# Performance work log

Measured on AMD Instinct MI355X. Metric: run time of the kernel, lower is better.

The kernel has to match this reference:

```python
import jax, jax.numpy as jnp
import numpy as np

RBF_START = 0.0
RBF_END = 10.0
RBF_STEPS = 64
OUT_SIZE = 64
ENERGY_SCALE = 0.1
P, L, R = 8, 128, 1024
COORD_SCALE = 5.0  # spread coords so pair distances span the 0-10 RBF range


def setup_inputs() -> dict:
    key = jax.random.key(0)
    k1, k2, k3, k4 = jax.random.split(key, 4)
    return {
        "lig_feat": jax.random.normal(k1, (L, RBF_STEPS, OUT_SIZE), dtype=jnp.float32),
        "rec_feat": jax.random.normal(k2, (R, RBF_STEPS, OUT_SIZE), dtype=jnp.float32),
        "lig_coords": jax.random.normal(k3, (P, L, 3), dtype=jnp.float32) * COORD_SCALE,
        "rec_coords": jax.random.normal(k4, (R, 3), dtype=jnp.float32) * COORD_SCALE,
    }


def reference(lig_feat, rec_feat, lig_coords, rec_coords):
    # attention coefficients: contract feature axis f -> [L, R, E]
    atn_coefs = jnp.einsum("lef,ref->lre", lig_feat, rec_feat)
    # pairwise distances for every pose: [P, L, R]
    diff = lig_coords[:, :, None, :] - rec_coords[None, None, :, :]
    dists = jnp.sqrt(jnp.sum(diff * diff, axis=-1))
    # RBF expansion: [P, L, R, E]
    mu = jnp.linspace(RBF_START, RBF_END, RBF_STEPS, dtype=jnp.float32)
    sigma = (RBF_START - RBF_END) / RBF_STEPS
    rbfs = jnp.exp(-(((dists[..., None] - mu) / sigma) ** 2))
    # attention-weighted energy per pose: [P]
    Us = jnp.einsum("plre,lre->p", rbfs, atn_coefs) * ENERGY_SCALE
    return Us
```

## Files before the change

kernel.cpp:

```cpp
#include <hip/hip_runtime.h>
#include <math.h>

#define Lc 128
#define Rc 1024
#define Pc 8
#define Ec 64
#define Fc 64

#define CSCALE   7.68718341623328f
#define MU_STEP  0.15873015873015873f
#define MUC      (MU_STEP * CSCALE)

#define BM 32
#define BN 32
#define EC 8
#define NBLKM ((Lc/BM)*(Rc/BN)*(Ec/EC))

typedef __attribute__((ext_vector_type(8))) short short8;
typedef __attribute__((ext_vector_type(4))) float f32x4;

__device__ __forceinline__ unsigned short bf16_rn(float x) {
    unsigned int u = __float_as_uint(x);
    u += 0x7FFF + ((u >> 16) & 1);
    return (unsigned short)(u >> 16);
}
__device__ __forceinline__ unsigned int hipack(float x0, float x1) {
    return (__float_as_uint(x0) >> 16) | (__float_as_uint(x1) & 0xFFFF0000u);
}
__device__ __forceinline__ unsigned int lopack(float x0, float x1) {
    float r0 = x0 - __uint_as_float(__float_as_uint(x0) & 0xFFFF0000u);
    float r1 = x1 - __uint_as_float(__float_as_uint(x1) & 0xFFFF0000u);
    return ((unsigned int)bf16_rn(r1) << 16) | (unsigned int)bf16_rn(r0);
}

__global__ __launch_bounds__(256, 2)
void ff_mfma(const float* __restrict__ lig_feat,
             const float* __restrict__ rec_feat,
             const float* __restrict__ lig_coords,
             const float* __restrict__ rec_coords,
             float* __restrict__ partial)
{
    __shared__ __align__(16) unsigned short stg[2][2][32][16][8];
    __shared__ float lcs[Pc][96];
    __shared__ float rcs[96];
    __shared__ float wred[4][Pc];

    const int tid  = threadIdx.x;
    const int lane = tid & 63;
    const int w    = tid >> 6;
    const int n16  = lane & 15;
    const int kg   = lane >> 4;
    const int sr   = w >> 1;
    const int sc   = w & 1;

    const int bid = blockIdx.x;
    const int loc = bid >> 3;
    const int rt  = (bid & 7) * 4 + (loc & 3);
    const int lt  = (loc >> 2) & 3;
    const int ez  = loc >> 4;
    const int r0  = rt * BN;
    const int l0  = lt * BM;
    const int e0  = ez * EC;

    for (int i = tid; i < Pc * 96; i += 256) {
        int p = i / 96, q = i - p * 96;
        lcs[p][q] = lig_coords[p * (Lc * 3) + l0 * 3 + q];
    }
    if (tid < 96) rcs[tid] = rec_coords[r0 * 3 + tid];
    __syncthreads();

    float dsc[Pc][4];
    {
        const int rb = (sc * 16 + n16) * 3;
        const float rx = rcs[rb], ry = rcs[rb + 1], rz = rcs[rb + 2];
        #pragma unroll
        for (int reg = 0; reg < 4; ++reg) {
            const int lb = (sr * 16 + kg * 4 + reg) * 3;
            #pragma unroll
            for (int p = 0; p < Pc; ++p) {
                float dx = lcs[p][lb]     - rx;
                float dy = lcs[p][lb + 1] - ry;
                float dz = lcs[p][lb + 2] - rz;
                dsc[p][reg] = sqrtf(dx * dx + dy * dy + dz * dz) * CSCALE;
            }
        }
    }

    const int half = tid >> 7;
    const int srow = (tid >> 2) & 31;
    const int fq   = tid & 3;
    const float* sbase = (half ? rec_feat + (size_t)(r0 + srow) * (Ec * Fc)
                               : lig_feat + (size_t)(l0 + srow) * (Ec * Fc)) + fq * 16;

    float4 pf[4];
    auto ld = [&](int e) {
        #pragma unroll
        for (int j = 0; j < 4; ++j)
            pf[j] = *(const float4*)(sbase + (size_t)e * Fc + j * 4);
    };
    auto cw = [&](int nb) {
        uint4 H0, H1, L0, L1;
        H0.x = hipack(pf[0].x, pf[0].y); H0.y = hipack(pf[0].z, pf[0].w);
        H0.z = hipack(pf[1].x, pf[1].y); H0.w = hipack(pf[1].z, pf[1].w);
        H1.x = hipack(pf[2].x, pf[2].y); H1.y = hipack(pf[2].z, pf[2].w);
        H1.z = hipack(pf[3].x, pf[3].y); H1.w = hipack(pf[3].z, pf[3].w);
        L0.x = lopack(pf[0].x, pf[0].y); L0.y = lopack(pf[0].z, pf[0].w);
        L0.z = lopack(pf[1].x, pf[1].y); L0.w = lopack(pf[1].z, pf[1].w);
        L1.x = lopack(pf[2].x, pf[2].y); L1.y = lopack(pf[2].z, pf[2].w);
        L1.z = lopack(pf[3].x, pf[3].y); L1.w = lopack(pf[3].z, pf[3].w);
        const int sm = srow & 15;
        *(uint4*)&stg[nb][half][srow][(fq * 2)         ^ sm][0] = H0;
        *(uint4*)&stg[nb][half][srow][(fq * 2 + 1)     ^ sm][0] = H1;
        *(uint4*)&stg[nb][half][srow][(8 + fq * 2)     ^ sm][0] = L0;
        *(uint4*)&stg[nb][half][srow][(8 + fq * 2 + 1) ^ sm][0] = L1;
    };

    ld(e0);
    cw(0);
    ld(e0 + 1);

    float us[Pc];
    #pragma unroll
    for (int p = 0; p < Pc; ++p) us[p] = 0.f;

    const int Arow = sr * 16 + n16;
    const int Brow = sc * 16 + n16;
#define RD(hf, rowv, slot) (*(const short8*)&stg[cur][hf][rowv][(slot) ^ ((rowv) & 15)][0])

    for (int t = 0; t < EC; ++t) {
        __syncthreads();
        const int cur = t & 1;

        f32x4 acc = {0.f, 0.f, 0.f, 0.f};
        {
            short8 a0 = RD(0, Arow, kg);
            short8 b0 = RD(1, Brow, kg);
            acc = __builtin_amdgcn_mfma_f32_16x16x32_bf16(a0, b0, acc, 0, 0, 0);
            short8 a1 = RD(0, Arow, 8 + kg);
            acc = __builtin_amdgcn_mfma_f32_16x16x32_bf16(a1, b0, acc, 0, 0, 0);
            short8 b1 = RD(1, Brow, 8 + kg);
            acc = __builtin_amdgcn_mfma_f32_16x16x32_bf16(a0, b1, acc, 0, 0, 0);
            a0 = RD(0, Arow, 4 + kg);
            b0 = RD(1, Brow, 4 + kg);
            acc = __builtin_amdgcn_mfma_f32_16x16x32_bf16(a0, b0, acc, 0, 0, 0);
            a1 = RD(0, Arow, 12 + kg);
            acc = __builtin_amdgcn_mfma_f32_16x16x32_bf16(a1, b0, acc, 0, 0, 0);
            b1 = RD(1, Brow, 12 + kg);
            acc = __builtin_amdgcn_mfma_f32_16x16x32_bf16(a0, b1, acc, 0, 0, 0);
        }

        const float musC = (float)(e0 + t) * MUC;
        #pragma unroll
        for (int reg = 0; reg < 4; ++reg) {
            const float av = acc[reg];
            #pragma unroll
            for (int p = 0; p < Pc; ++p) {
                const float tt = dsc[p][reg] - musC;
                us[p] = fmaf(av, __builtin_amdgcn_exp2f(-tt * tt), us[p]);
            }
        }

        if (t + 1 < EC) cw((t + 1) & 1);
        if (t + 2 < EC) ld(e0 + t + 2);
    }
#undef RD

    #pragma unroll
    for (int p = 0; p < Pc; ++p) {
        float v = us[p];
        #pragma unroll
        for (int off = 32; off >= 1; off >>= 1)
            v += __shfl_xor(v, off, 64);
        us[p] = v;
    }
    if (lane == 0) {
        #pragma unroll
        for (int p = 0; p < Pc; ++p) wred[w][p] = us[p];
    }
    __syncthreads();
    if (tid < Pc) {
        float s = 0.f;
        #pragma unroll
        for (int k = 0; k < 4; ++k) s += wred[k][tid];
        partial[(size_t)bid * Pc + tid] = s;
    }
}

__global__ void ff_reduce(const float* __restrict__ partial, float* __restrict__ out)
{
    const int w    = threadIdx.x >> 6;
    const int lane = threadIdx.x & 63;
    float v = 0.f;
    #pragma unroll
    for (int j = 0; j < NBLKM / 64; ++j)
        v += partial[(size_t)(lane + 64 * j) * Pc + w];
    #pragma unroll
    for (int off = 32; off >= 1; off >>= 1)
        v += __shfl_xor(v, off, 64);
    if (lane == 0) out[w] = 0.1f * v;
}

extern "C" void kernel_launch(void* const* d_in, const int* in_sizes, int n_in,
                              void* d_out, int out_size, void* d_ws, size_t ws_size,
                              hipStream_t stream)
{
    const float* lig_feat   = (const float*)d_in[0];
    const float* rec_feat   = (const float*)d_in[1];
    const float* lig_coords = (const float*)d_in[2];
    const float* rec_coords = (const float*)d_in[3];
    float* out     = (float*)d_out;
    float* partial = (float*)d_ws;

    ff_mfma<<<NBLKM, 256, 0, stream>>>(lig_feat, rec_feat, lig_coords, rec_coords, partial);
    ff_reduce<<<1, 512, 0, stream>>>(partial, out);
}
```

Baseline: 33.64 us.

## Skip negligible RBF terms per tile and fuse final reduction via last-block atomic

Computes per-wave min/max scaled distance for each pose and skips the MFMA and exp work for RBF centers whose Gaussian contribution is below about 2^-42 across the whole tile. It also replaces the separate reduce kernel with a last-block-done pattern using an atomic counter, reset by a memset before launch. The skip adds branching and reductions up front and only helps when a tile's distance range is narrow. The memset adds its own launch, which offsets part of what is saved by dropping the reduce kernel.

Result: slower. 93.07 us (+176.7%).

```diff
diff --git a/kernel.cpp b/kernel.cpp
--- a/kernel.cpp
+++ b/kernel.cpp
@@ -10,6 +10,7 @@
 #define CSCALE   7.68718341623328f
 #define MU_STEP  0.15873015873015873f
 #define MUC      (MU_STEP * CSCALE)
+#define SKIP_THR 6.5f
 
 #define BM 32
 #define BN 32
@@ -38,12 +39,15 @@
              const float* __restrict__ rec_feat,
              const float* __restrict__ lig_coords,
              const float* __restrict__ rec_coords,
-             float* __restrict__ partial)
+             float* __restrict__ partial,
+             int* __restrict__ counter,
+             float* __restrict__ out)
 {
     __shared__ __align__(16) unsigned short stg[2][2][32][16][8];
     __shared__ float lcs[Pc][96];
     __shared__ float rcs[96];
     __shared__ float wred[4][Pc];
+    __shared__ int lastBlk;
 
     const int tid  = threadIdx.x;
     const int lane = tid & 63;
@@ -84,6 +88,20 @@
                 dsc[p][reg] = sqrtf(dx * dx + dy * dy + dz * dz) * CSCALE;
             }
         }
+    }
+
+    unsigned sminb[Pc], smaxb[Pc];
+    #pragma unroll
+    for (int p = 0; p < Pc; ++p) {
+        float mn = fminf(fminf(dsc[p][0], dsc[p][1]), fminf(dsc[p][2], dsc[p][3]));
+        float mx = fmaxf(fmaxf(dsc[p][0], dsc[p][1]), fmaxf(dsc[p][2], dsc[p][3]));
+        #pragma unroll
+        for (int off = 32; off >= 1; off >>= 1) {
+            mn = fminf(mn, __shfl_xor(mn, off, 64));
+            mx = fmaxf(mx, __shfl_xor(mx, off, 64));
+        }
+        sminb[p] = __builtin_amdgcn_readfirstlane(__float_as_uint(mn));
+        smaxb[p] = __builtin_amdgcn_readfirstlane(__float_as_uint(mx));
     }
 
     const int half = tid >> 7;
@@ -130,9 +148,20 @@
     for (int t = 0; t < EC; ++t) {
         __syncthreads();
         const int cur = t & 1;
+        const float musC = (float)(e0 + t) * MUC;
+
+        bool act[Pc];
+        bool any = false;
+        #pragma unroll
+        for (int p = 0; p < Pc; ++p) {
+            const float mn = __uint_as_float(sminb[p]);
+            const float mx = __uint_as_float(smaxb[p]);
+            act[p] = (mn - musC <= SKIP_THR) && (mx - musC >= -SKIP_THR);
+            any = any || act[p];
+        }
 
         f32x4 acc = {0.f, 0.f, 0.f, 0.f};
-        {
+        if (any) {
             short8 a0 = RD(0, Arow, kg);
             short8 b0 = RD(1, Brow, kg);
             acc = __builtin_amdgcn_mfma_f32_16x16x32_bf16(a0, b0, acc, 0, 0, 0);
@@ -147,16 +176,16 @@
             acc = __builtin_amdgcn_mfma_f32_16x16x32_bf16(a1, b0, acc, 0, 0, 0);
             b1 = RD(1, Brow, 12 + kg);
             acc = __builtin_amdgcn_mfma_f32_16x16x32_bf16(a0, b1, acc, 0, 0, 0);
-        }
-
-        const float musC = (float)(e0 + t) * MUC;
-        #pragma unroll
-        for (int reg = 0; reg < 4; ++reg) {
-            const float av = acc[reg];
+
             #pragma unroll
             for (int p = 0; p < Pc; ++p) {
-                const float tt = dsc[p][reg] - musC;
-                us[p] = fmaf(av, __builtin_amdgcn_exp2f(-tt * tt), us[p]);
+                if (act[p]) {
+                    #pragma unroll
+                    for (int reg = 0; reg < 4; ++reg) {
+                        const float tt = dsc[p][reg] - musC;
+                        us[p] = fmaf(acc[reg], __builtin_amdgcn_exp2f(-tt * tt), us[p]);
+                    }
+                }
             }
         }
 
@@ -184,20 +213,27 @@
         for (int k = 0; k < 4; ++k) s += wred[k][tid];
         partial[(size_t)bid * Pc + tid] = s;
     }
-}
-
-__global__ void ff_reduce(const float* __restrict__ partial, float* __restrict__ out)
-{
-    const int w    = threadIdx.x >> 6;
-    const int lane = threadIdx.x & 63;
-    float v = 0.f;
-    #pragma unroll
-    for (int j = 0; j < NBLKM / 64; ++j)
-        v += partial[(size_t)(lane + 64 * j) * Pc + w];
-    #pragma unroll
-    for (int off = 32; off >= 1; off >>= 1)
-        v += __shfl_xor(v, off, 64);
-    if (lane == 0) out[w] = 0.1f * v;
+
+    __threadfence();
+    if (tid == 0)
+        lastBlk = (atomicAdd(counter, 1) == NBLKM - 1);
+    __syncthreads();
+    if (lastBlk) {
+        __threadfence();
+        float v = 0.f;
+        #pragma unroll
+        for (int j = 0; j < NBLKM * Pc / 256; ++j)
+            v += partial[tid + 256 * j];
+        float* red2 = &lcs[0][0];
+        red2[tid] = v;
+        __syncthreads();
+        if (tid < Pc) {
+            float s = 0.f;
+            #pragma unroll
+            for (int k = 0; k < 32; ++k) s += red2[k * Pc + tid];
+            out[tid] = 0.1f * s;
+        }
+    }
 }
 
 extern "C" void kernel_launch(void* const* d_in, const int* in_sizes, int n_in,
@@ -210,7 +246,9 @@
     const float* rec_coords = (const float*)d_in[3];
     float* out     = (float*)d_out;
     float* partial = (float*)d_ws;
-
-    ff_mfma<<<NBLKM, 256, 0, stream>>>(lig_feat, rec_feat, lig_coords, rec_coords, partial);
-    ff_reduce<<<1, 512, 0, stream>>>(partial, out);
-}
+    int*   counter = (int*)((char*)d_ws + 32768);
+
+    hipMemsetAsync(counter, 0, sizeof(int), stream);
+    ff_mfma<<<NBLKM, 256, 0, stream>>>(lig_feat, rec_feat, lig_coords, rec_coords,
+                                       partial, counter, out);
+}
```

## Stage operands per wave in private LDS to drop block-wide barriers

Applied to the files above, without the earlier changes.

Each wave now loads and converts its own 16 ligand rows and 16 receptor rows into a wave-private LDS slot. This removes the per-iteration __syncthreads and the double-buffer indexing. The bf16 hi/lo conversion and the next prefetch are moved ahead of the exp/FMA epilogue so they overlap with it. In exchange, each feature row is now fetched by two waves instead of one, which doubles global/L2 load traffic and raises per-thread prefetch registers.

Result: slower. 48.36 us (+43.7%).

```diff
diff --git a/kernel.cpp b/kernel.cpp
--- a/kernel.cpp
+++ b/kernel.cpp
@@ -40,7 +40,7 @@
              const float* __restrict__ rec_coords,
              float* __restrict__ partial)
 {
-    __shared__ __align__(16) unsigned short stg[2][2][32][16][8];
+    __shared__ __align__(16) unsigned short stg[4][2][16][16][8];
     __shared__ float lcs[Pc][96];
     __shared__ float rcs[96];
     __shared__ float wred[4][Pc];
@@ -86,68 +86,67 @@
         }
     }
 
-    const int half = tid >> 7;
-    const int srow = (tid >> 2) & 31;
-    const int fq   = tid & 3;
-    const float* sbase = (half ? rec_feat + (size_t)(r0 + srow) * (Ec * Fc)
-                               : lig_feat + (size_t)(l0 + srow) * (Ec * Fc)) + fq * 16;
-
-    float4 pf[4];
+    const int half = lane >> 5;
+    const int srow = (lane >> 1) & 15;
+    const int fq   = lane & 1;
+    const int grow = half ? (r0 + sc * 16 + srow) : (l0 + sr * 16 + srow);
+    const float* sbase = (half ? rec_feat : lig_feat)
+                         + (size_t)grow * (Ec * Fc) + fq * 32;
+
+    float4 pf[8];
     auto ld = [&](int e) {
         #pragma unroll
-        for (int j = 0; j < 4; ++j)
+        for (int j = 0; j < 8; ++j)
             pf[j] = *(const float4*)(sbase + (size_t)e * Fc + j * 4);
     };
-    auto cw = [&](int nb) {
-        uint4 H0, H1, L0, L1;
-        H0.x = hipack(pf[0].x, pf[0].y); H0.y = hipack(pf[0].z, pf[0].w);
-        H0.z = hipack(pf[1].x, pf[1].y); H0.w = hipack(pf[1].z, pf[1].w);
-        H1.x = hipack(pf[2].x, pf[2].y); H1.y = hipack(pf[2].z, pf[2].w);
-        H1.z = hipack(pf[3].x, pf[3].y); H1.w = hipack(pf[3].z, pf[3].w);
-        L0.x = lopack(pf[0].x, pf[0].y); L0.y = lopack(pf[0].z, pf[0].w);
-        L0.z = lopack(pf[1].x, pf[1].y); L0.w = lopack(pf[1].z, pf[1].w);
-        L1.x = lopack(pf[2].x, pf[2].y); L1.y = lopack(pf[2].z, pf[2].w);
-        L1.z = lopack(pf[3].x, pf[3].y); L1.w = lopack(pf[3].z, pf[3].w);
-        const int sm = srow & 15;
-        *(uint4*)&stg[nb][half][srow][(fq * 2)         ^ sm][0] = H0;
-        *(uint4*)&stg[nb][half][srow][(fq * 2 + 1)     ^ sm][0] = H1;
-        *(uint4*)&stg[nb][half][srow][(8 + fq * 2)     ^ sm][0] = L0;
-        *(uint4*)&stg[nb][half][srow][(8 + fq * 2 + 1) ^ sm][0] = L1;
+    auto cw = [&]() {
+        #pragma unroll
+        for (int k = 0; k < 4; ++k) {
+            uint4 H, L;
+            H.x = hipack(pf[2 * k].x,     pf[2 * k].y);
+            H.y = hipack(pf[2 * k].z,     pf[2 * k].w);
+            H.z = hipack(pf[2 * k + 1].x, pf[2 * k + 1].y);
+            H.w = hipack(pf[2 * k + 1].z, pf[2 * k + 1].w);
+            L.x = lopack(pf[2 * k].x,     pf[2 * k].y);
+            L.y = lopack(pf[2 * k].z,     pf[2 * k].w);
+            L.z = lopack(pf[2 * k + 1].x, pf[2 * k + 1].y);
+            L.w = lopack(pf[2 * k + 1].z, pf[2 * k + 1].w);
+            *(uint4*)&stg[w][half][srow][(fq * 4 + k) ^ srow][0]       = H;
+            *(uint4*)&stg[w][half][srow][((8 + fq * 4 + k)) ^ srow][0] = L;
+        }
     };
 
     ld(e0);
-    cw(0);
+    cw();
     ld(e0 + 1);
 
     float us[Pc];
     #pragma unroll
     for (int p = 0; p < Pc; ++p) us[p] = 0.f;
 
-    const int Arow = sr * 16 + n16;
-    const int Brow = sc * 16 + n16;
-#define RD(hf, rowv, slot) (*(const short8*)&stg[cur][hf][rowv][(slot) ^ ((rowv) & 15)][0])
+#define RD(hf, slot) (*(const short8*)&stg[w][hf][n16][(slot) ^ n16][0])
 
     for (int t = 0; t < EC; ++t) {
-        __syncthreads();
-        const int cur = t & 1;
-
         f32x4 acc = {0.f, 0.f, 0.f, 0.f};
         {
-            short8 a0 = RD(0, Arow, kg);
-            short8 b0 = RD(1, Brow, kg);
+            short8 a0 = RD(0, kg);
+            short8 b0 = RD(1, kg);
             acc = __builtin_amdgcn_mfma_f32_16x16x32_bf16(a0, b0, acc, 0, 0, 0);
-            short8 a1 = RD(0, Arow, 8 + kg);
+            short8 a1 = RD(0, 8 + kg);
             acc = __builtin_amdgcn_mfma_f32_16x16x32_bf16(a1, b0, acc, 0, 0, 0);
-            short8 b1 = RD(1, Brow, 8 + kg);
+            short8 b1 = RD(1, 8 + kg);
             acc = __builtin_amdgcn_mfma_f32_16x16x32_bf16(a0, b1, acc, 0, 0, 0);
-            a0 = RD(0, Arow, 4 + kg);
-            b0 = RD(1, Brow, 4 + kg);
+            a0 = RD(0, 4 + kg);
+            b0 = RD(1, 4 + kg);
             acc = __builtin_amdgcn_mfma_f32_16x16x32_bf16(a0, b0, acc, 0, 0, 0);
-            a1 = RD(0, Arow, 12 + kg);
+            a1 = RD(0, 12 + kg);
             acc = __builtin_amdgcn_mfma_f32_16x16x32_bf16(a1, b0, acc, 0, 0, 0);
-            b1 = RD(1, Brow, 12 + kg);
+            b1 = RD(1, 12 + kg);
             acc = __builtin_amdgcn_mfma_f32_16x16x32_bf16(a0, b1, acc, 0, 0, 0);
         }
+
+        if (t + 1 < EC) cw();
+        if (t + 2 < EC) ld(e0 + t + 2);
 
         const float musC = (float)(e0 + t) * MUC;
         #pragma unroll
@@ -159,9 +158,6 @@
                 us[p] = fmaf(av, __builtin_amdgcn_exp2f(-tt * tt), us[p]);
             }
         }
-
-        if (t + 1 < EC) cw((t + 1) & 1);
-        if (t + 2 < EC) ld(e0 + t + 2);
     }
 #undef RD
 
```
